# Performance work log

Measured on AMD Instinct MI355X. Metric: run time of the kernel, lower is better.

The kernel has to match this reference:

```python
import jax, jax.numpy as jnp
import numpy as np

T, N = 12, 1000          # frames, pedestrians
RNN, EMB, GS, OUT = 128, 64, 4, 5
G = GS * GS              # 16 grid cells


def lstm_cell(x, h, c, W_ih, W_hh, b_ih, b_hh):
    # PyTorch LSTMCell gate order: i, f, g, o
    gates = x @ W_ih.T + h @ W_hh.T + b_ih + b_hh
    i, f, g, o = jnp.split(gates, 4, axis=-1)
    c_new = jax.nn.sigmoid(f) * c + jax.nn.sigmoid(i) * jnp.tanh(g)
    h_new = jax.nn.sigmoid(o) * jnp.tanh(c_new)
    return h_new, c_new


def setup_inputs() -> dict:
    key = jax.random.key(0)
    ks = jax.random.split(key, 10)
    s = 0.02  # small init scale for weights
    # binary occupancy grid masks: grid[f, n, p, g] = 1 if ped p falls in cell g of ped n's neighborhood
    grids = (jax.random.uniform(ks[1], (T, N, N, G)) < 0.02).astype(jnp.float32)
    return {
        "input_data": jax.random.normal(ks[0], (T, N, 2), dtype=jnp.float32),
        "grids": grids,
        "hidden_states": jnp.zeros((N, RNN), dtype=jnp.float32),
        "cell_states": jnp.zeros((N, RNN), dtype=jnp.float32),
        "W_in": jax.random.normal(ks[2], (EMB, 2)) * s,
        "b_in": jnp.zeros((EMB,), dtype=jnp.float32),
        "W_soc": jax.random.normal(ks[3], (EMB, G * RNN)) * s,
        "b_soc": jnp.zeros((EMB,), dtype=jnp.float32),
        "W_ih": jax.random.normal(ks[4], (4 * RNN, 2 * EMB)) * s,
        "W_hh": jax.random.normal(ks[5], (4 * RNN, RNN)) * s,
        "b_ih": jnp.zeros((4 * RNN,), dtype=jnp.float32),
        "b_hh": jnp.zeros((4 * RNN,), dtype=jnp.float32),
        "W_out": jax.random.normal(ks[6], (OUT, RNN)) * s,
        "b_out": jnp.zeros((OUT,), dtype=jnp.float32),
    }


def reference(input_data, grids, hidden_states, cell_states,
              W_in, b_in, W_soc, b_soc, W_ih, W_hh, b_ih, b_hh, W_out, b_out):
    def step(carry, frame):
        h, c = carry
        x, grid = frame  # x: [N,2], grid: [N,N,G]
        # social pooling: for each node n, grid[n].T @ h  -> [G, RNN]
        social = jnp.einsum('npg,ph->ngh', grid, h).reshape(N, G * RNN)
        ie = jax.nn.relu(x @ W_in.T + b_in)           # [N, EMB]
        te = jax.nn.relu(social @ W_soc.T + b_soc)    # [N, EMB]
        emb = jnp.concatenate([ie, te], axis=-1)      # [N, 2*EMB]
        h, c = lstm_cell(emb, h, c, W_ih, W_hh, b_ih, b_hh)
        out = h @ W_out.T + b_out                     # [N, OUT]
        return (h, c), out

    (h, c), outputs = jax.lax.scan(step, (hidden_states, cell_states),
                                   (input_data, grids))
    return outputs, h, c  # outputs: [T, N, OUT]
```

## Files before the change

### kernel.cpp

```cpp
#include <hip/hip_runtime.h>


#define TT    12
#define NN    1000
#define RNNW  128
#define OUTD  5
#define GROW  16000
#define UCW   1024

__device__ __forceinline__ float sigmf(float x) { return 1.f / (1.f + __expf(-x)); }

__global__ void k_prep(const float* __restrict__ h0, const float* __restrict__ c0,
                       const float* __restrict__ W_soc,
                       const float* __restrict__ W_ih, const float* __restrict__ W_hh,
                       float* __restrict__ h, float* __restrict__ c,
                       float* __restrict__ WsT2p, float* __restrict__ WcT2p) {
    int i = blockIdx.x * 256 + threadIdx.x;
    if (i < 131072) {
        int e = i >> 11, gk = i & 2047, g = gk >> 7, k = gk & 127;
        int j = g * 64 + e;
        WsT2p[(k >> 1) * 2048 + j * 2 + (k & 1)] = W_soc[i];
    } else if (i < 196608) {
        int i2 = i - 131072;
        int j = i2 >> 7, k = i2 & 127;
        WcT2p[(k >> 1) * 1024 + j * 2 + (k & 1)] = W_ih[i2];
    } else if (i < 262144) {
        int i3 = i - 196608;
        int j = i3 >> 7, k = i3 & 127;
        WcT2p[((k >> 1) + 64) * 1024 + j * 2 + (k & 1)] = W_hh[i3];
    } else if (i < 262144 + NN * RNNW) {
        int i4 = i - 262144; h[i4] = h0[i4];
    } else if (i < 262144 + 2 * NN * RNNW) {
        int i5 = i - 262144 - NN * RNNW; c[i5] = c0[i5];
    }
}

__device__ __forceinline__ void compute_U(const float (*sH)[RNNW],
                                          const float* __restrict__ WsT2p,
                                          float* __restrict__ U, int n0, int tid) {
    const int jd = tid;
    float acc0[4] = {0.f, 0.f, 0.f, 0.f};
    float acc1[4] = {0.f, 0.f, 0.f, 0.f};
    for (int k = 0; k < RNNW; k += 4) {
        float4 a[4];
        #pragma unroll
        for (int p = 0; p < 4; ++p) a[p] = *(const float4*)(&sH[p][k]);
        const int r0 = (k >> 1), r1 = (k >> 1) + 1;
        float2 w00 = *(const float2*)(WsT2p + r0 * 2048 + jd * 2);
        float2 w01 = *(const float2*)(WsT2p + r0 * 2048 + (jd + 512) * 2);
        float2 w10 = *(const float2*)(WsT2p + r1 * 2048 + jd * 2);
        float2 w11 = *(const float2*)(WsT2p + r1 * 2048 + (jd + 512) * 2);
        #pragma unroll
        for (int p = 0; p < 4; ++p) {
            acc0[p] += a[p].x * w00.x + a[p].y * w00.y + a[p].z * w10.x + a[p].w * w10.y;
            acc1[p] += a[p].x * w01.x + a[p].y * w01.y + a[p].z * w11.x + a[p].w * w11.y;
        }
    }
    #pragma unroll
    for (int p = 0; p < 4; ++p) {
        U[(size_t)(n0 + p) * UCW + jd]       = acc0[p];
        U[(size_t)(n0 + p) * UCW + jd + 512] = acc1[p];
    }
}

__global__ __launch_bounds__(512) void k_U0(const float* __restrict__ h,
                                            const float* __restrict__ WsT2p,
                                            float* __restrict__ U) {
    __shared__ float sH[4][RNNW];
    const int tid = threadIdx.x, n0 = blockIdx.x * 4;
    { int pl = tid >> 7, r = tid & 127; sH[pl][r] = h[(size_t)(n0 + pl) * RNNW + r]; }
    __syncthreads();
    compute_U(sH, WsT2p, U, n0, tid);
}

__global__ __launch_bounds__(512) void k_pool(const unsigned int* __restrict__ grids,
                                              const float* __restrict__ x_in,
                                              const float* __restrict__ U,
                                              const float* __restrict__ W_in,
                                              const float* __restrict__ b_in,
                                              const float* __restrict__ b_soc,
                                              float* __restrict__ A, int t) {
    const int n = blockIdx.x;
    const int tid = threadIdx.x;
    const int lane = tid & 63, wave = tid >> 6;
    const unsigned int* gp = grids + ((size_t)t * NN + n) * (size_t)GROW;
    float acc = 0.f;
    for (int it = 0; it < 8; ++it) {
        int base = (it * 8 + wave) * 256;
        if (base >= GROW) break;
        int f0 = base + lane * 4;
        uint4 v = {0u, 0u, 0u, 0u};
        if (f0 < GROW) v = *(const uint4*)(gp + f0);
        unsigned int va[4] = {v.x, v.y, v.z, v.w};
        #pragma unroll
        for (int sub = 0; sub < 4; ++sub) {
            unsigned long long m = __ballot(va[sub] != 0u);
            while (m) {
                int b = __builtin_ctzll(m); m &= m - 1;
                int f = base + b * 4 + sub;
                acc += U[(size_t)(f >> 4) * UCW + (f & 15) * 64 + lane];
            }
        }
    }
    __shared__ float sAcc[8][64];
    sAcc[wave][lane] = acc;
    __syncthreads();
    if (tid < 64) {
        float s = 0.f;
        #pragma unroll
        for (int w = 0; w < 8; w++) s += sAcc[w][tid];
        float te = fmaxf(s + b_soc[tid], 0.f);
        float x0 = x_in[((size_t)t * NN + n) * 2 + 0];
        float x1 = x_in[((size_t)t * NN + n) * 2 + 1];
        float ie = fmaxf(W_in[tid * 2 + 0] * x0 + W_in[tid * 2 + 1] * x1 + b_in[tid], 0.f);
        A[(size_t)n * RNNW + tid]      = ie;
        A[(size_t)n * RNNW + 64 + tid] = te;
    }
}

__global__ __launch_bounds__(512) void k_cell(const float* __restrict__ A,
                                              float* __restrict__ h, float* __restrict__ c,
                                              const float* __restrict__ WcT2p,
                                              const float* __restrict__ WsT2p,
                                              const float* __restrict__ b_ih,
                                              const float* __restrict__ b_hh,
                                              const float* __restrict__ W_out,
                                              const float* __restrict__ b_out,
                                              float* __restrict__ U,
                                              float* __restrict__ out, int t, int doU) {
    __shared__ float sA[4][RNNW], sH[4][RNNW], sC[4][RNNW];
    __shared__ float sG[4][512];
    __shared__ float sRed[4][2][OUTD];
    const int tid = threadIdx.x;
    const int lane = tid & 63;
    const int n0 = blockIdx.x * 4;
    {
        int pl = tid >> 7, r = tid & 127;
        sA[pl][r] = A[(size_t)(n0 + pl) * RNNW + r];
        sH[pl][r] = h[(size_t)(n0 + pl) * RNNW + r];
        sC[pl][r] = c[(size_t)(n0 + pl) * RNNW + r];
    }
    __syncthreads();
    {
        const int jh = tid & 255, ph = tid >> 8;
        float g00 = 0.f, g01 = 0.f, g10 = 0.f, g11 = 0.f;
        #pragma unroll 4
        for (int k = 0; k < 128; k += 4) {
            float4 aA = *(const float4*)(&sA[2 * ph][k]);
            float4 aB = *(const float4*)(&sA[2 * ph + 1][k]);
            const int r0 = (k >> 1), r1 = (k >> 1) + 1;
            float2 w00 = *(const float2*)(WcT2p + r0 * 1024 + jh * 2);
            float2 w01 = *(const float2*)(WcT2p + r0 * 1024 + (jh + 256) * 2);
            float2 w10 = *(const float2*)(WcT2p + r1 * 1024 + jh * 2);
            float2 w11 = *(const float2*)(WcT2p + r1 * 1024 + (jh + 256) * 2);
            g00 += aA.x * w00.x + aA.y * w00.y + aA.z * w10.x + aA.w * w10.y;
            g01 += aA.x * w01.x + aA.y * w01.y + aA.z * w11.x + aA.w * w11.y;
            g10 += aB.x * w00.x + aB.y * w00.y + aB.z * w10.x + aB.w * w10.y;
            g11 += aB.x * w01.x + aB.y * w01.y + aB.z * w11.x + aB.w * w11.y;
        }
        #pragma unroll 4
        for (int k = 0; k < 128; k += 4) {
            float4 aA = *(const float4*)(&sH[2 * ph][k]);
            float4 aB = *(const float4*)(&sH[2 * ph + 1][k]);
            const int r0 = 64 + (k >> 1), r1 = 64 + (k >> 1) + 1;
            float2 w00 = *(const float2*)(WcT2p + r0 * 1024 + jh * 2);
            float2 w01 = *(const float2*)(WcT2p + r0 * 1024 + (jh + 256) * 2);
            float2 w10 = *(const float2*)(WcT2p + r1 * 1024 + jh * 2);
            float2 w11 = *(const float2*)(WcT2p + r1 * 1024 + (jh + 256) * 2);
            g00 += aA.x * w00.x + aA.y * w00.y + aA.z * w10.x + aA.w * w10.y;
            g01 += aA.x * w01.x + aA.y * w01.y + aA.z * w11.x + aA.w * w11.y;
            g10 += aB.x * w00.x + aB.y * w00.y + aB.z * w10.x + aB.w * w10.y;
            g11 += aB.x * w01.x + aB.y * w01.y + aB.z * w11.x + aB.w * w11.y;
        }
        float bias0 = b_ih[jh] + b_hh[jh];
        float bias1 = b_ih[jh + 256] + b_hh[jh + 256];
        sG[2 * ph][jh]           = g00 + bias0;
        sG[2 * ph][jh + 256]     = g01 + bias1;
        sG[2 * ph + 1][jh]       = g10 + bias0;
        sG[2 * ph + 1][jh + 256] = g11 + bias1;
    }
    __syncthreads();
    {
        int pl = tid >> 7, r = tid & 127;
        float gi = sG[pl][r], gf = sG[pl][128 + r];
        float gg = sG[pl][256 + r], go = sG[pl][384 + r];
        float cn = sigmf(gf) * sC[pl][r] + sigmf(gi) * tanhf(gg);
        float hn = sigmf(go) * tanhf(cn);
        sC[pl][r] = cn;
        sH[pl][r] = hn;
        c[(size_t)(n0 + pl) * RNNW + r] = cn;
        h[(size_t)(n0 + pl) * RNNW + r] = hn;
    }
    __syncthreads();
    {
        int pl = tid >> 7, p128 = tid & 127, wh = (tid >> 6) & 1;
        float v = sH[pl][p128];
        #pragma unroll
        for (int d = 0; d < OUTD; ++d) {
            float pr = v * W_out[d * RNNW + p128];
            #pragma unroll
            for (int off = 32; off > 0; off >>= 1) pr += __shfl_down(pr, off);
            if (lane == 0) sRed[pl][wh][d] = pr;
        }
    }
    __syncthreads();
    if (tid < 4 * OUTD) {
        int pl = tid / OUTD, d = tid % OUTD;
        out[((size_t)t * NN + n0 + pl) * OUTD + d] =
            sRed[pl][0][d] + sRed[pl][1][d] + b_out[d];
    }
    if (doU) compute_U(sH, WsT2p, U, n0, tid);
}

__global__ void k_final(const float* __restrict__ h, const float* __restrict__ c,
                        float* __restrict__ out) {
    int i = blockIdx.x * 256 + threadIdx.x;
    if (i < NN * RNNW) {
        out[TT * NN * OUTD + i] = h[i];
        out[TT * NN * OUTD + NN * RNNW + i] = c[i];
    }
}

extern "C" void kernel_launch(void* const* d_in, const int* in_sizes, int n_in,
                              void* d_out, int out_size, void* d_ws, size_t ws_size,
                              hipStream_t stream) {
    const float* x_in       = (const float*)d_in[0];
    const unsigned int* grd = (const unsigned int*)d_in[1];
    const float* h0         = (const float*)d_in[2];
    const float* c0         = (const float*)d_in[3];
    const float* W_in       = (const float*)d_in[4];
    const float* b_in       = (const float*)d_in[5];
    const float* W_soc      = (const float*)d_in[6];
    const float* b_soc      = (const float*)d_in[7];
    const float* W_ih       = (const float*)d_in[8];
    const float* W_hh       = (const float*)d_in[9];
    const float* b_ih       = (const float*)d_in[10];
    const float* b_hh       = (const float*)d_in[11];
    const float* W_out      = (const float*)d_in[12];
    const float* b_out      = (const float*)d_in[13];
    float* out = (float*)d_out;

    float* h      = (float*)d_ws;
    float* c      = h + NN * RNNW;
    float* U      = c + NN * RNNW;
    float* A      = U + (size_t)NN * UCW;
    float* WsT2p  = A + (size_t)NN * RNNW;
    float* WcT2p  = WsT2p + 131072;

    hipLaunchKernelGGL(k_prep, dim3(2024), dim3(256), 0, stream,
                       h0, c0, W_soc, W_ih, W_hh, h, c, WsT2p, WcT2p);
    hipLaunchKernelGGL(k_U0, dim3(250), dim3(512), 0, stream, h, WsT2p, U);
    for (int t = 0; t < TT; ++t) {
        hipLaunchKernelGGL(k_pool, dim3(NN), dim3(512), 0, stream,
                           grd, x_in, U, W_in, b_in, b_soc, A, t);
        hipLaunchKernelGGL(k_cell, dim3(250), dim3(512), 0, stream,
                           A, h, c, WcT2p, WsT2p, b_ih, b_hh, W_out, b_out,
                           U, out, t, (t < TT - 1) ? 1 : 0);
    }
    hipLaunchKernelGGL(k_final, dim3(500), dim3(256), 0, stream, h, c, out);
}
```

Measured before the change: 712.0 us.

## Pre-pack all grid frames into bitmasks in one upfront kernel

Adds a k_pack kernel that reads the whole float occupancy grid once, for all frames, and stores ballot bitmasks (252 u64 words per row). The per-step k_pool kernel then reads these compact masks instead of scanning 64 KB per row. The grid stream is still read in full, but now by one large, highly parallel launch instead of twelve launches that sit on the serial recurrence. The pool kernels become light. This costs an extra mask write and read and one more launch.

```diff
diff --git a/kernel.cpp b/kernel.cpp
--- a/kernel.cpp
+++ b/kernel.cpp
@@ -7,6 +7,8 @@
 #define OUTD  5
 #define GROW  16000
 #define UCW   1024
+#define NCHK  63
+#define WPR   252
 
 __device__ __forceinline__ float sigmf(float x) { return 1.f / (1.f + __expf(-x)); }
 
@@ -35,6 +37,29 @@
     }
 }
 
+__global__ __launch_bounds__(512) void k_pack(const unsigned int* __restrict__ grd,
+                                              unsigned long long* __restrict__ mask) {
+    const int row = blockIdx.x;
+    const int lane = threadIdx.x & 63, wave = threadIdx.x >> 6;
+    const unsigned int* gp = grd + (size_t)row * GROW;
+    unsigned long long* mrow = mask + (size_t)row * WPR;
+    for (int it = 0; it < 8; ++it) {
+        int c = it * 8 + wave;
+        if (c >= NCHK) break;
+        int f0 = c * 256 + lane * 4;
+        uint4 v = {0u, 0u, 0u, 0u};
+        if (f0 < GROW) v = *(const uint4*)(gp + f0);
+        unsigned long long m0 = __ballot(v.x != 0u);
+        unsigned long long m1 = __ballot(v.y != 0u);
+        unsigned long long m2 = __ballot(v.z != 0u);
+        unsigned long long m3 = __ballot(v.w != 0u);
+        if (lane < 4) {
+            unsigned long long w = (lane == 0) ? m0 : (lane == 1) ? m1 : (lane == 2) ? m2 : m3;
+            mrow[c * 4 + lane] = w;
+        }
+    }
+}
+
 __device__ __forceinline__ void compute_U(const float (*sH)[RNNW],
                                           const float* __restrict__ WsT2p,
                                           float* __restrict__ U, int n0, int tid) {
@@ -73,7 +98,7 @@
     compute_U(sH, WsT2p, U, n0, tid);
 }
 
-__global__ __launch_bounds__(512) void k_pool(const unsigned int* __restrict__ grids,
+__global__ __launch_bounds__(512) void k_pool(const unsigned long long* __restrict__ mask,
                                               const float* __restrict__ x_in,
                                               const float* __restrict__ U,
                                               const float* __restrict__ W_in,
@@ -83,18 +108,15 @@
     const int n = blockIdx.x;
     const int tid = threadIdx.x;
     const int lane = tid & 63, wave = tid >> 6;
-    const unsigned int* gp = grids + ((size_t)t * NN + n) * (size_t)GROW;
+    const unsigned long long* mrow = mask + (size_t)(t * NN + n) * WPR;
     float acc = 0.f;
     for (int it = 0; it < 8; ++it) {
-        int base = (it * 8 + wave) * 256;
-        if (base >= GROW) break;
-        int f0 = base + lane * 4;
-        uint4 v = {0u, 0u, 0u, 0u};
-        if (f0 < GROW) v = *(const uint4*)(gp + f0);
-        unsigned int va[4] = {v.x, v.y, v.z, v.w};
+        int c = it * 8 + wave;
+        if (c >= NCHK) break;
+        const int base = c * 256;
         #pragma unroll
         for (int sub = 0; sub < 4; ++sub) {
-            unsigned long long m = __ballot(va[sub] != 0u);
+            unsigned long long m = mrow[c * 4 + sub];
             while (m) {
                 int b = __builtin_ctzll(m); m &= m - 1;
                 int f = base + b * 4 + sub;
@@ -246,13 +268,15 @@
     float* A      = U + (size_t)NN * UCW;
     float* WsT2p  = A + (size_t)NN * RNNW;
     float* WcT2p  = WsT2p + 131072;
+    unsigned long long* mask = (unsigned long long*)(WcT2p + 131072);
 
     hipLaunchKernelGGL(k_prep, dim3(2024), dim3(256), 0, stream,
                        h0, c0, W_soc, W_ih, W_hh, h, c, WsT2p, WcT2p);
+    hipLaunchKernelGGL(k_pack, dim3(TT * NN), dim3(512), 0, stream, grd, mask);
     hipLaunchKernelGGL(k_U0, dim3(250), dim3(512), 0, stream, h, WsT2p, U);
     for (int t = 0; t < TT; ++t) {
         hipLaunchKernelGGL(k_pool, dim3(NN), dim3(512), 0, stream,
-                           grd, x_in, U, W_in, b_in, b_soc, A, t);
+                           mask, x_in, U, W_in, b_in, b_soc, A, t);
         hipLaunchKernelGGL(k_cell, dim3(250), dim3(512), 0, stream,
                            A, h, c, WcT2p, WsT2p, b_ih, b_hh, W_out, b_out,
                            U, out, t, (t < TT - 1) ? 1 : 0);
```

After: 847.8 us. 19.1% more time.

## Fuse social pooling into LSTM cell kernel with double-buffered U

Applied to the files above, without the earlier changes.

Merges the per-frame pooling and LSTM cell kernels into one step kernel. Each 512-thread block handles 4 pedestrians, two waves per pedestrian, and prefetches grid chunks four deep. Sparse gathers are split over four independent accumulators. U is double-buffered so a block can write next-frame U while other blocks still read the current one, and the final h/c copy kernel is folded into the last step. This removes half the launches and the A round trip through global memory, but it cuts the pooling grid from 1000 blocks to 250, which lowers parallelism for the grid-streaming part.

```diff
diff --git a/kernel.cpp b/kernel.cpp
--- a/kernel.cpp
+++ b/kernel.cpp
@@ -7,6 +7,7 @@
 #define OUTD  5
 #define GROW  16000
 #define UCW   1024
+#define NCHK  63
 
 __device__ __forceinline__ float sigmf(float x) { return 1.f / (1.f + __expf(-x)); }
 
@@ -73,72 +74,88 @@
     compute_U(sH, WsT2p, U, n0, tid);
 }
 
-__global__ __launch_bounds__(512) void k_pool(const unsigned int* __restrict__ grids,
-                                              const float* __restrict__ x_in,
-                                              const float* __restrict__ U,
-                                              const float* __restrict__ W_in,
-                                              const float* __restrict__ b_in,
-                                              const float* __restrict__ b_soc,
-                                              float* __restrict__ A, int t) {
-    const int n = blockIdx.x;
-    const int tid = threadIdx.x;
-    const int lane = tid & 63, wave = tid >> 6;
-    const unsigned int* gp = grids + ((size_t)t * NN + n) * (size_t)GROW;
-    float acc = 0.f;
-    for (int it = 0; it < 8; ++it) {
-        int base = (it * 8 + wave) * 256;
-        if (base >= GROW) break;
-        int f0 = base + lane * 4;
-        uint4 v = {0u, 0u, 0u, 0u};
-        if (f0 < GROW) v = *(const uint4*)(gp + f0);
-        unsigned int va[4] = {v.x, v.y, v.z, v.w};
-        #pragma unroll
-        for (int sub = 0; sub < 4; ++sub) {
-            unsigned long long m = __ballot(va[sub] != 0u);
-            while (m) {
-                int b = __builtin_ctzll(m); m &= m - 1;
-                int f = base + b * 4 + sub;
-                acc += U[(size_t)(f >> 4) * UCW + (f & 15) * 64 + lane];
-            }
-        }
-    }
+__global__ __launch_bounds__(512) void k_step(
+    const unsigned int* __restrict__ grd, const float* __restrict__ x_in,
+    const float* __restrict__ Uin, float* __restrict__ Uout,
+    float* __restrict__ h, float* __restrict__ c,
+    const float* __restrict__ WcT2p, const float* __restrict__ WsT2p,
+    const float* __restrict__ W_in, const float* __restrict__ b_in,
+    const float* __restrict__ b_soc,
+    const float* __restrict__ b_ih, const float* __restrict__ b_hh,
+    const float* __restrict__ W_out, const float* __restrict__ b_out,
+    float* __restrict__ out, int t, int doU)
+{
     __shared__ float sAcc[8][64];
-    sAcc[wave][lane] = acc;
-    __syncthreads();
-    if (tid < 64) {
-        float s = 0.f;
-        #pragma unroll
-        for (int w = 0; w < 8; w++) s += sAcc[w][tid];
-        float te = fmaxf(s + b_soc[tid], 0.f);
-        float x0 = x_in[((size_t)t * NN + n) * 2 + 0];
-        float x1 = x_in[((size_t)t * NN + n) * 2 + 1];
-        float ie = fmaxf(W_in[tid * 2 + 0] * x0 + W_in[tid * 2 + 1] * x1 + b_in[tid], 0.f);
-        A[(size_t)n * RNNW + tid]      = ie;
-        A[(size_t)n * RNNW + 64 + tid] = te;
-    }
-}
-
-__global__ __launch_bounds__(512) void k_cell(const float* __restrict__ A,
-                                              float* __restrict__ h, float* __restrict__ c,
-                                              const float* __restrict__ WcT2p,
-                                              const float* __restrict__ WsT2p,
-                                              const float* __restrict__ b_ih,
-                                              const float* __restrict__ b_hh,
-                                              const float* __restrict__ W_out,
-                                              const float* __restrict__ b_out,
-                                              float* __restrict__ U,
-                                              float* __restrict__ out, int t, int doU) {
     __shared__ float sA[4][RNNW], sH[4][RNNW], sC[4][RNNW];
     __shared__ float sG[4][512];
     __shared__ float sRed[4][2][OUTD];
     const int tid = threadIdx.x;
     const int lane = tid & 63;
     const int n0 = blockIdx.x * 4;
-    {
-        int pl = tid >> 7, r = tid & 127;
-        sA[pl][r] = A[(size_t)(n0 + pl) * RNNW + r];
-        sH[pl][r] = h[(size_t)(n0 + pl) * RNNW + r];
-        sC[pl][r] = c[(size_t)(n0 + pl) * RNNW + r];
+
+    { int pl = tid >> 7, r = tid & 127;
+      sH[pl][r] = h[(size_t)(n0 + pl) * RNNW + r];
+      sC[pl][r] = c[(size_t)(n0 + pl) * RNNW + r]; }
+
+    {
+        const int wv = tid >> 6, pl = wv >> 1, half = wv & 1;
+        const unsigned int* gp = grd + (size_t)(t * NN + n0 + pl) * GROW;
+        float ac0 = 0.f, ac1 = 0.f, ac2 = 0.f, ac3 = 0.f;
+        uint4 buf[4];
+        #pragma unroll
+        for (int q = 0; q < 4; ++q) {
+            int cq = q * 2 + half;
+            int f0 = cq * 256 + lane * 4;
+            buf[q] = make_uint4(0u, 0u, 0u, 0u);
+            if (cq < NCHK && f0 < GROW) buf[q] = *(const uint4*)(gp + f0);
+        }
+        for (int it = 0; it < 32; ++it) {
+            const int cc = it * 2 + half;
+            if (cc >= NCHK) break;
+            uint4 cur = buf[it & 3];
+            {
+                int itn = it + 4;
+                if (itn < 32) {
+                    int cn = itn * 2 + half;
+                    int f0 = cn * 256 + lane * 4;
+                    uint4 nv = make_uint4(0u, 0u, 0u, 0u);
+                    if (cn < NCHK && f0 < GROW) nv = *(const uint4*)(gp + f0);
+                    buf[it & 3] = nv;
+                }
+            }
+            unsigned long long m0 = __ballot(cur.x != 0u);
+            unsigned long long m1 = __ballot(cur.y != 0u);
+            unsigned long long m2 = __ballot(cur.z != 0u);
+            unsigned long long m3 = __ballot(cur.w != 0u);
+            const int base = cc * 256;
+            while (m0 | m1 | m2 | m3) {
+                float u0 = 0.f, u1 = 0.f, u2 = 0.f, u3 = 0.f;
+                if (m0) { int b = __builtin_ctzll(m0); m0 &= m0 - 1;
+                          int f = base + b * 4 + 0;
+                          u0 = Uin[(size_t)(f >> 4) * UCW + (f & 15) * 64 + lane]; }
+                if (m1) { int b = __builtin_ctzll(m1); m1 &= m1 - 1;
+                          int f = base + b * 4 + 1;
+                          u1 = Uin[(size_t)(f >> 4) * UCW + (f & 15) * 64 + lane]; }
+                if (m2) { int b = __builtin_ctzll(m2); m2 &= m2 - 1;
+                          int f = base + b * 4 + 2;
+                          u2 = Uin[(size_t)(f >> 4) * UCW + (f & 15) * 64 + lane]; }
+                if (m3) { int b = __builtin_ctzll(m3); m3 &= m3 - 1;
+                          int f = base + b * 4 + 3;
+                          u3 = Uin[(size_t)(f >> 4) * UCW + (f & 15) * 64 + lane]; }
+                ac0 += u0; ac1 += u1; ac2 += u2; ac3 += u3;
+            }
+        }
+        sAcc[wv][lane] = (ac0 + ac1) + (ac2 + ac3);
+    }
+    __syncthreads();
+    if (tid < 256) {
+        int pl = tid >> 6, e = tid & 63;
+        float te = fmaxf(sAcc[2 * pl][e] + sAcc[2 * pl + 1][e] + b_soc[e], 0.f);
+        float x0 = x_in[(size_t)(t * NN + n0 + pl) * 2 + 0];
+        float x1 = x_in[(size_t)(t * NN + n0 + pl) * 2 + 1];
+        float ie = fmaxf(W_in[e * 2 + 0] * x0 + W_in[e * 2 + 1] * x1 + b_in[e], 0.f);
+        sA[pl][e]      = ie;
+        sA[pl][64 + e] = te;
     }
     __syncthreads();
     {
@@ -190,6 +207,10 @@
         sH[pl][r] = hn;
         c[(size_t)(n0 + pl) * RNNW + r] = cn;
         h[(size_t)(n0 + pl) * RNNW + r] = hn;
+        if (t == TT - 1) {
+            out[(size_t)TT * NN * OUTD + (size_t)(n0 + pl) * RNNW + r] = hn;
+            out[(size_t)TT * NN * OUTD + (size_t)NN * RNNW + (size_t)(n0 + pl) * RNNW + r] = cn;
+        }
     }
     __syncthreads();
     {
@@ -209,16 +230,7 @@
         out[((size_t)t * NN + n0 + pl) * OUTD + d] =
             sRed[pl][0][d] + sRed[pl][1][d] + b_out[d];
     }
-    if (doU) compute_U(sH, WsT2p, U, n0, tid);
-}
-
-__global__ void k_final(const float* __restrict__ h, const float* __restrict__ c,
-                        float* __restrict__ out) {
-    int i = blockIdx.x * 256 + threadIdx.x;
-    if (i < NN * RNNW) {
-        out[TT * NN * OUTD + i] = h[i];
-        out[TT * NN * OUTD + NN * RNNW + i] = c[i];
-    }
+    if (doU) compute_U(sH, WsT2p, Uout, n0, tid);
 }
 
 extern "C" void kernel_launch(void* const* d_in, const int* in_sizes, int n_in,
@@ -242,20 +254,20 @@
 
     float* h      = (float*)d_ws;
     float* c      = h + NN * RNNW;
-    float* U      = c + NN * RNNW;
-    float* A      = U + (size_t)NN * UCW;
-    float* WsT2p  = A + (size_t)NN * RNNW;
+    float* U0b    = c + NN * RNNW;
+    float* U1b    = U0b + (size_t)NN * UCW;
+    float* WsT2p  = U1b + (size_t)NN * UCW;
     float* WcT2p  = WsT2p + 131072;
 
     hipLaunchKernelGGL(k_prep, dim3(2024), dim3(256), 0, stream,
                        h0, c0, W_soc, W_ih, W_hh, h, c, WsT2p, WcT2p);
-    hipLaunchKernelGGL(k_U0, dim3(250), dim3(512), 0, stream, h, WsT2p, U);
+    hipLaunchKernelGGL(k_U0, dim3(250), dim3(512), 0, stream, h, WsT2p, U0b);
     for (int t = 0; t < TT; ++t) {
-        hipLaunchKernelGGL(k_pool, dim3(NN), dim3(512), 0, stream,
-                           grd, x_in, U, W_in, b_in, b_soc, A, t);
-        hipLaunchKernelGGL(k_cell, dim3(250), dim3(512), 0, stream,
-                           A, h, c, WcT2p, WsT2p, b_ih, b_hh, W_out, b_out,
-                           U, out, t, (t < TT - 1) ? 1 : 0);
-    }
-    hipLaunchKernelGGL(k_final, dim3(500), dim3(256), 0, stream, h, c, out);
-}
+        float* Uin  = (t & 1) ? U1b : U0b;
+        float* Uout = (t & 1) ? U0b : U1b;
+        hipLaunchKernelGGL(k_step, dim3(250), dim3(512), 0, stream,
+                           grd, x_in, Uin, Uout, h, c, WcT2p, WsT2p,
+                           W_in, b_in, b_soc, b_ih, b_hh, W_out, b_out,
+                           out, t, (t < TT - 1) ? 1 : 0);
+    }
+}
```

Measured after the change: 1.137 ms. 1.6x slower.
